# Kernel optimization log

Measured on AMD Instinct MI355X. Metric: run time of the kernel, lower is better.

## Reference

```python
import jax, jax.numpy as jnp
import numpy as np

N = 50000      # nodes
E = 800000     # edges
D = 96         # nfeat
C = 40         # nclass
NITE = 8       # train_nite / eval_nite
SMOOTH = 0.5   # smooth_fac


def setup_inputs() -> dict:
    key = jax.random.key(0)
    ks = jax.random.split(key, 6)
    x = jax.random.normal(ks[0], (N, D), dtype=jnp.float32)
    edge_row = jax.random.randint(ks[1], (E,), 0, N)
    edge_col = jax.random.randint(ks[2], (E,), 0, N)
    # ~1/avg_degree scale mimics a symmetrically normalized adjacency
    edge_vals = jax.random.uniform(ks[3], (E,), dtype=jnp.float32) / 16.0
    W_gc = jax.random.normal(ks[4], (D, D), dtype=jnp.float32) / jnp.sqrt(jnp.float32(D))
    b_gc = jnp.zeros((D,), dtype=jnp.float32)
    W_lin = jax.random.normal(ks[5], (D, C), dtype=jnp.float32) / jnp.sqrt(jnp.float32(D))
    return {"x": x, "edge_row": edge_row, "edge_col": edge_col,
            "edge_vals": edge_vals, "W_gc": W_gc, "b_gc": b_gc, "W_lin": W_lin}


def reference(x, edge_row, edge_col, edge_vals, W_gc, b_gc, W_lin):
    # One iteration: GraphConvolution (support = h @ W; out = A @ support + b),
    # smoothing skip connection, ReLU. Dropout is identity (eval / rate 0).
    def one_iter(h, _):
        support = h @ W_gc                                   # [N, D]
        msg = support[edge_col] * edge_vals[:, None]         # [E, D] gather + scale
        agg = jax.ops.segment_sum(msg, edge_row, num_segments=N) + b_gc  # [N, D]
        h_new = jax.nn.relu(SMOOTH * h + (1.0 - SMOOTH) * agg)
        return h_new, None

    h, _ = jax.lax.scan(one_iter, x, None, length=NITE)
    logits = h @ W_lin                                       # [N, C]
    return jax.nn.log_softmax(logits, axis=1)
```

## Files before the change

### kernel.cpp

```cpp
#include <hip/hip_runtime.h>

#define N_NODES 50000
#define E_EDGES 800000
#define D_FEAT  96
#define C_CLS   40
#define N_ITER  8

#define SCAN_CHUNK 1024
#define SCAN_NB ((N_NODES + SCAN_CHUNK - 1) / SCAN_CHUNK)

typedef short bf16x8 __attribute__((ext_vector_type(8)));
typedef float f32x4  __attribute__((ext_vector_type(4)));
typedef float f32x2  __attribute__((ext_vector_type(2)));

#if defined(__has_builtin)
#if __has_builtin(__builtin_amdgcn_cvt_pk_f32_fp8) && __has_builtin(__builtin_amdgcn_cvt_pk_fp8_f32)
#define HAVE_FP8_CVT 1
#endif
#endif
#ifndef HAVE_FP8_CVT
#define HAVE_FP8_CVT 0
#endif

static __device__ __forceinline__ unsigned short f2bf(float f) {
    unsigned u = __float_as_uint(f);
    u = (u + 0x7FFF + ((u >> 16) & 1)) >> 16;
    return (unsigned short)u;
}

static __device__ __forceinline__ unsigned f32_to_fp8_manual(float f) {
    unsigned u = __float_as_uint(f);
    unsigned s = u >> 31;
    int e8 = (int)((u >> 23) & 0xFF) - 127 + 7;
    unsigned m23 = u & 0x7FFFFF;
    if (e8 <= 0) return s << 7;
    if (e8 >= 15) return (s << 7) | 0x7E;
    unsigned m = m23 >> 20;
    unsigned rem = m23 & 0xFFFFF;
    if (rem > 0x80000u || (rem == 0x80000u && (m & 1))) {
        m++;
        if (m == 8) { m = 0; e8++; if (e8 >= 15) return (s << 7) | 0x7E; }
    }
    return (s << 7) | ((unsigned)e8 << 3) | m;
}
static __device__ __forceinline__ float fp8_to_f32_manual(unsigned b) {
    unsigned s = (b >> 7) & 1, e = (b >> 3) & 0xF, m = b & 7;
    if (e == 0) return 0.0f;
    return __uint_as_float((s << 31) | ((e + 120) << 23) | (m << 20));
}

static __device__ __forceinline__ void fp8x4_dec(unsigned w, float* o) {
#if HAVE_FP8_CVT
    f32x2 lo = __builtin_amdgcn_cvt_pk_f32_fp8(w, false);
    f32x2 hi = __builtin_amdgcn_cvt_pk_f32_fp8(w, true);
    o[0] = lo[0]; o[1] = lo[1]; o[2] = hi[0]; o[3] = hi[1];
#else
    o[0] = fp8_to_f32_manual(w & 0xFF);
    o[1] = fp8_to_f32_manual((w >> 8) & 0xFF);
    o[2] = fp8_to_f32_manual((w >> 16) & 0xFF);
    o[3] = fp8_to_f32_manual((w >> 24) & 0xFF);
#endif
}
static __device__ __forceinline__ unsigned fp8x4_enc(float a, float b, float c, float d) {
#if HAVE_FP8_CVT
    unsigned w = __builtin_amdgcn_cvt_pk_fp8_f32(a, b, 0, false);
    w = __builtin_amdgcn_cvt_pk_fp8_f32(c, d, (int)w, true);
    return w;
#else
    return f32_to_fp8_manual(a) | (f32_to_fp8_manual(b) << 8) |
           (f32_to_fp8_manual(c) << 16) | (f32_to_fp8_manual(d) << 24);
#endif
}

__global__ __launch_bounds__(256) void k_hist(const int* __restrict__ erow,
                                              int* __restrict__ deg) {
    int e = blockIdx.x * 256 + threadIdx.x;
    if (e >= E_EDGES) return;
    atomicAdd(&deg[erow[e]], 1);
}

__global__ __launch_bounds__(256) void k_scan_reduce(const int* __restrict__ deg,
                                                     int* __restrict__ bsum) {
    __shared__ int sbuf[256];
    int tid = threadIdx.x;
    int base = blockIdx.x * SCAN_CHUNK + tid * 4;
    int s = 0;
    #pragma unroll
    for (int j = 0; j < 4; ++j) {
        int idx = base + j;
        if (idx < N_NODES) s += deg[idx];
    }
    sbuf[tid] = s;
    __syncthreads();
    for (int d = 128; d > 0; d >>= 1) {
        if (tid < d) sbuf[tid] += sbuf[tid + d];
        __syncthreads();
    }
    if (tid == 0) bsum[blockIdx.x] = sbuf[0];
}

__global__ __launch_bounds__(64) void k_scan_tops(int* __restrict__ bsum) {
    int lane = threadIdx.x;
    int v = (lane < SCAN_NB) ? bsum[lane] : 0;
    int inc = v;
    #pragma unroll
    for (int d = 1; d < 64; d <<= 1) {
        int up = __shfl_up(inc, d, 64);
        if (lane >= d) inc += up;
    }
    if (lane < SCAN_NB) bsum[lane] = inc - v;
}

__global__ __launch_bounds__(256) void k_scan_add(const int* __restrict__ deg,
                                                  const int* __restrict__ bsum_ex,
                                                  int* __restrict__ off,
                                                  int* __restrict__ cursor) {
    __shared__ int sbuf[256];
    int tid = threadIdx.x;
    int base = blockIdx.x * SCAN_CHUNK + tid * 4;
    int v[4];
    int s = 0;
    #pragma unroll
    for (int j = 0; j < 4; ++j) {
        int idx = base + j;
        v[j] = (idx < N_NODES) ? deg[idx] : 0;
        s += v[j];
    }
    sbuf[tid] = s;
    __syncthreads();
    for (int d = 1; d < 256; d <<= 1) {
        int t = (tid >= d) ? sbuf[tid - d] : 0;
        __syncthreads();
        sbuf[tid] += t;
        __syncthreads();
    }
    int ex = bsum_ex[blockIdx.x] + sbuf[tid] - s;
    #pragma unroll
    for (int j = 0; j < 4; ++j) {
        int idx = base + j;
        if (idx < N_NODES) {
            off[idx] = ex;
            cursor[idx] = ex;
            ex += v[j];
        }
    }
    if (blockIdx.x == 0 && tid == 0) off[N_NODES] = E_EDGES;
}

__global__ __launch_bounds__(256) void k_build(const int* __restrict__ erow,
                                               const int* __restrict__ ecol,
                                               const float* __restrict__ eval_,
                                               int* __restrict__ cursor,
                                               unsigned* __restrict__ epk) {
    int e = blockIdx.x * 256 + threadIdx.x;
    if (e >= E_EDGES) return;
    int r = erow[e];
    int pos = atomicAdd(&cursor[r], 1);
    unsigned pk = (unsigned)(ecol[e] & 0xFFFF) | ((unsigned)f2bf(eval_[e]) << 16);
    epk[pos] = pk;
}

__global__ __launch_bounds__(256) void k_prep_w(const float* __restrict__ W,
                                                unsigned short* __restrict__ WB) {
    for (int idx = threadIdx.x; idx < 18 * 64; idx += 256) {
        int grp = idx >> 6;
        int lane = idx & 63;
        int t = grp / 3, s = grp - t * 3;
        int n = t * 16 + (lane & 15);
        int k0 = s * 32 + (lane >> 4) * 8;
        unsigned short* dst = WB + (size_t)idx * 8;
        #pragma unroll
        for (int j = 0; j < 8; ++j)
            dst[j] = f2bf(W[(k0 + j) * D_FEAT + n]);
    }
}

__global__ __launch_bounds__(256) void k_cvt_bf16(const float* __restrict__ src,
                                                  unsigned short* __restrict__ dst,
                                                  int n8) {
    int g = blockIdx.x * 256 + threadIdx.x;
    if (g >= n8) return;
    const float4* s4 = (const float4*)src + (size_t)g * 2;
    float4 x0 = s4[0], x1 = s4[1];
    float vals[8] = {x0.x, x0.y, x0.z, x0.w, x1.x, x1.y, x1.z, x1.w};
    uint4 pk; unsigned* pku = (unsigned*)&pk;
    #pragma unroll
    for (int w2 = 0; w2 < 4; ++w2) {
        unsigned lo = f2bf(vals[w2 * 2 + 0]);
        unsigned hi = f2bf(vals[w2 * 2 + 1]);
        pku[w2] = lo | (hi << 16);
    }
    *(uint4*)(dst + (size_t)g * 8) = pk;
}

__global__ __launch_bounds__(256) void k_matmul_mfma(
        const unsigned short* __restrict__ hb,
        const unsigned short* __restrict__ WB,
        unsigned char* __restrict__ support) {
    __shared__ float sm[64 * 100];
    int tid = threadIdx.x;
    int wave = tid >> 6, lane = tid & 63;
    int q = lane >> 4, c = lane & 15;
    int m0 = blockIdx.x * 64 + wave * 16;

    if (m0 < N_NODES) {
        const unsigned short* arow = hb + (size_t)(m0 + c) * D_FEAT + q * 8;
        bf16x8 a0 = *(const bf16x8*)(arow);
        bf16x8 a1 = *(const bf16x8*)(arow + 32);
        bf16x8 a2 = *(const bf16x8*)(arow + 64);
        #pragma unroll
        for (int t = 0; t < 6; ++t) {
            const unsigned short* bp = WB + ((size_t)(t * 3) * 64 + lane) * 8;
            bf16x8 b0 = *(const bf16x8*)(bp);
            bf16x8 b1 = *(const bf16x8*)(bp + 64 * 8);
            bf16x8 b2 = *(const bf16x8*)(bp + 128 * 8);
            f32x4 acc = {0.f, 0.f, 0.f, 0.f};
            acc = __builtin_amdgcn_mfma_f32_16x16x32_bf16(a0, b0, acc, 0, 0, 0);
            acc = __builtin_amdgcn_mfma_f32_16x16x32_bf16(a1, b1, acc, 0, 0, 0);
            acc = __builtin_amdgcn_mfma_f32_16x16x32_bf16(a2, b2, acc, 0, 0, 0);
            #pragma unroll
            for (int r = 0; r < 4; ++r)
                sm[(wave * 16 + q * 4 + r) * 100 + t * 16 + c] = acc[r];
        }
    }
    __syncthreads();

    #pragma unroll
    for (int oo = 0; oo < 3; ++oo) {
        int o = tid + oo * 256;
        int row = o / 12;
        int cb = (o - row * 12) * 8;
        int grow = blockIdx.x * 64 + row;
        if (grow < N_NODES) {
            const float* sp = sm + row * 100 + cb;
            uint2 pk;
            pk.x = fp8x4_enc(sp[0], sp[1], sp[2], sp[3]);
            pk.y = fp8x4_enc(sp[4], sp[5], sp[6], sp[7]);
            *(uint2*)(support + (size_t)grow * D_FEAT + cb) = pk;
        }
    }
}

__global__ __launch_bounds__(192) void k_agg(const int* __restrict__ off,
                                             const unsigned* __restrict__ epk,
                                             const unsigned char* __restrict__ support,
                                             const unsigned short* hin,
                                             const float* __restrict__ b,
                                             unsigned short* hout) {
    int gid = blockIdx.x * 192 + threadIdx.x;
    int n = gid / 12;
    int q = gid % 12;
    if (n >= N_NODES) return;

    int s = off[n];
    int e = off[n + 1];

    float acc[8];
    #pragma unroll
    for (int j = 0; j < 8; ++j) acc[j] = 0.0f;

    int i = s;
    for (; i < e && (i & 3); ++i) {
        unsigned p = epk[i];
        float v = __uint_as_float(p & 0xFFFF0000u);
        uint2 r = *(const uint2*)(support + (size_t)(p & 0xFFFFu) * D_FEAT + q * 8);
        float f[8];
        fp8x4_dec(r.x, f);
        fp8x4_dec(r.y, f + 4);
        #pragma unroll
        for (int j = 0; j < 8; ++j) acc[j] = fmaf(f[j], v, acc[j]);
    }
    for (; i + 4 <= e; i += 4) {
        uint4 pq = *(const uint4*)(epk + i);
        const unsigned* pp = (const unsigned*)&pq;
        uint2 r0 = *(const uint2*)(support + (size_t)(pp[0] & 0xFFFFu) * D_FEAT + q * 8);
        uint2 r1 = *(const uint2*)(support + (size_t)(pp[1] & 0xFFFFu) * D_FEAT + q * 8);
        uint2 r2 = *(const uint2*)(support + (size_t)(pp[2] & 0xFFFFu) * D_FEAT + q * 8);
        uint2 r3 = *(const uint2*)(support + (size_t)(pp[3] & 0xFFFFu) * D_FEAT + q * 8);
        float v0 = __uint_as_float(pp[0] & 0xFFFF0000u);
        float v1 = __uint_as_float(pp[1] & 0xFFFF0000u);
        float v2 = __uint_as_float(pp[2] & 0xFFFF0000u);
        float v3 = __uint_as_float(pp[3] & 0xFFFF0000u);
        float f0[8], f1[8], f2[8], f3[8];
        fp8x4_dec(r0.x, f0); fp8x4_dec(r0.y, f0 + 4);
        fp8x4_dec(r1.x, f1); fp8x4_dec(r1.y, f1 + 4);
        fp8x4_dec(r2.x, f2); fp8x4_dec(r2.y, f2 + 4);
        fp8x4_dec(r3.x, f3); fp8x4_dec(r3.y, f3 + 4);
        #pragma unroll
        for (int j = 0; j < 8; ++j) {
            acc[j] = fmaf(f0[j], v0, acc[j]);
            acc[j] = fmaf(f1[j], v1, acc[j]);
            acc[j] = fmaf(f2[j], v2, acc[j]);
            acc[j] = fmaf(f3[j], v3, acc[j]);
        }
    }
    for (; i < e; ++i) {
        unsigned p = epk[i];
        float v = __uint_as_float(p & 0xFFFF0000u);
        uint2 r = *(const uint2*)(support + (size_t)(p & 0xFFFFu) * D_FEAT + q * 8);
        float f[8];
        fp8x4_dec(r.x, f);
        fp8x4_dec(r.y, f + 4);
        #pragma unroll
        for (int j = 0; j < 8; ++j) acc[j] = fmaf(f[j], v, acc[j]);
    }

    uint4 hq = *(const uint4*)(hin + (size_t)n * D_FEAT + q * 8);
    const unsigned* hu = (const unsigned*)&hq;
    const float* brow = b + q * 8;
    float og[8];
    #pragma unroll
    for (int w2 = 0; w2 < 4; ++w2) {
        float h0 = __uint_as_float(hu[w2] << 16);
        float h1 = __uint_as_float(hu[w2] & 0xFFFF0000u);
        og[w2*2+0] = fmaxf(0.5f * h0 + 0.5f * (acc[w2*2+0] + brow[w2*2+0]), 0.0f);
        og[w2*2+1] = fmaxf(0.5f * h1 + 0.5f * (acc[w2*2+1] + brow[w2*2+1]), 0.0f);
    }
    uint4 pk; unsigned* pku = (unsigned*)&pk;
    #pragma unroll
    for (int w2 = 0; w2 < 4; ++w2) {
        unsigned lo = f2bf(og[w2 * 2 + 0]);
        unsigned hi = f2bf(og[w2 * 2 + 1]);
        pku[w2] = lo | (hi << 16);
    }
    *(uint4*)(hout + (size_t)n * D_FEAT + q * 8) = pk;
}

__global__ __launch_bounds__(256) void k_final(const unsigned short* __restrict__ hb,
                                               const float* __restrict__ Wg,
                                               float* __restrict__ out) {
    __shared__ float Wl[D_FEAT * C_CLS];
    {
        const float4* src = (const float4*)Wg;
        float4* dst = (float4*)Wl;
        for (int i = threadIdx.x; i < 960; i += 256) dst[i] = src[i];
    }
    __syncthreads();

    int n = blockIdx.x * 256 + threadIdx.x;
    if (n >= N_NODES) return;

    float acc[C_CLS];
    #pragma unroll
    for (int c = 0; c < C_CLS; ++c) acc[c] = 0.0f;

    const unsigned short* hrow = hb + (size_t)n * D_FEAT;
    for (int g = 0; g < 12; ++g) {
        uint4 hq = *(const uint4*)(hrow + g * 8);
        const unsigned* hu = (const unsigned*)&hq;
        float hv[8];
        #pragma unroll
        for (int w2 = 0; w2 < 4; ++w2) {
            hv[w2*2+0] = __uint_as_float(hu[w2] << 16);
            hv[w2*2+1] = __uint_as_float(hu[w2] & 0xFFFF0000u);
        }
        #pragma unroll
        for (int kk = 0; kk < 8; ++kk) {
            float hs = hv[kk];
            const float* wr = &Wl[(g * 8 + kk) * C_CLS];
            #pragma unroll
            for (int c4 = 0; c4 < 10; ++c4) {
                float4 w = *(const float4*)(wr + c4 * 4);
                acc[c4 * 4 + 0] = fmaf(hs, w.x, acc[c4 * 4 + 0]);
                acc[c4 * 4 + 1] = fmaf(hs, w.y, acc[c4 * 4 + 1]);
                acc[c4 * 4 + 2] = fmaf(hs, w.z, acc[c4 * 4 + 2]);
                acc[c4 * 4 + 3] = fmaf(hs, w.w, acc[c4 * 4 + 3]);
            }
        }
    }

    float m = acc[0];
    #pragma unroll
    for (int c = 1; c < C_CLS; ++c) m = fmaxf(m, acc[c]);
    float s = 0.0f;
    #pragma unroll
    for (int c = 0; c < C_CLS; ++c) s += expf(acc[c] - m);
    float lse = m + logf(s);

    float* orow = out + (size_t)n * C_CLS;
    #pragma unroll
    for (int c4 = 0; c4 < 10; ++c4)
        *(float4*)(orow + c4 * 4) =
            make_float4(acc[c4 * 4 + 0] - lse, acc[c4 * 4 + 1] - lse,
                        acc[c4 * 4 + 2] - lse, acc[c4 * 4 + 3] - lse);
}

static inline size_t align256(size_t x) { return (x + 255) & ~(size_t)255; }

extern "C" void kernel_launch(void* const* d_in, const int* in_sizes, int n_in,
                              void* d_out, int out_size, void* d_ws, size_t ws_size,
                              hipStream_t stream) {
    const float* x    = (const float*)d_in[0];
    const int*   erow = (const int*)  d_in[1];
    const int*   ecol = (const int*)  d_in[2];
    const float* ev   = (const float*)d_in[3];
    const float* Wgc  = (const float*)d_in[4];
    const float* bgc  = (const float*)d_in[5];
    const float* Wlin = (const float*)d_in[6];
    float* out = (float*)d_out;

    const size_t NF = (size_t)N_NODES * D_FEAT;
    char* ws = (char*)d_ws;
    unsigned short* hb         = (unsigned short*)ws; ws += align256(NF * 2);
    unsigned short* xb         = (unsigned short*)ws; ws += align256(NF * 2);
    unsigned char*  support_f8 = (unsigned char*)ws;  ws += align256(NF);
    unsigned*       epk        = (unsigned*)ws;       ws += align256((size_t)E_EDGES * 4);
    unsigned short* WB         = (unsigned short*)ws; ws += align256((size_t)18 * 64 * 8 * 2);
    int*            off        = (int*)ws;            ws += align256((size_t)(N_NODES + 1) * 4);
    int*            deg        = (int*)ws;            ws += align256((size_t)N_NODES * 4);
    int*            cursor     = (int*)ws;            ws += align256((size_t)N_NODES * 4);
    int*            bsum       = (int*)ws;            ws += align256((size_t)SCAN_NB * 4);

    hipMemsetAsync(deg, 0, (size_t)N_NODES * 4, stream);
    k_prep_w     <<<1, 256, 0, stream>>>(Wgc, WB);
    k_cvt_bf16   <<<(int)((NF / 8 + 255) / 256), 256, 0, stream>>>(x, xb, (int)(NF / 8));
    k_hist       <<<(E_EDGES + 255) / 256, 256, 0, stream>>>(erow, deg);
    k_scan_reduce<<<SCAN_NB, 256, 0, stream>>>(deg, bsum);
    k_scan_tops  <<<1, 64, 0, stream>>>(bsum);
    k_scan_add   <<<SCAN_NB, 256, 0, stream>>>(deg, bsum, off, cursor);
    k_build      <<<(E_EDGES + 255) / 256, 256, 0, stream>>>(erow, ecol, ev, cursor, epk);

    const int g_mm = (N_NODES + 63) / 64;
    const int g_ag = (N_NODES * 12 + 191) / 192;
    for (int it = 0; it < N_ITER; ++it) {
        const unsigned short* hin = (it == 0) ? xb : hb;
        k_matmul_mfma<<<g_mm, 256, 0, stream>>>(hin, WB, support_f8);
        k_agg        <<<g_ag, 192, 0, stream>>>(off, epk, support_f8, hin, bgc, hb);
    }
    k_final<<<(N_NODES + 255) / 256, 256, 0, stream>>>(hb, Wlin, out);
}
```

Measured before the change: 442.7 us.

## Sort nodes by degree for aggregation and widen per-thread feature slice to 16

Adds a degree histogram, scan and scatter that build a permutation grouping nodes of equal in-degree, so wavefronts in the aggregation kernel process nodes with similar edge counts and diverge less. The aggregation kernel now uses 6 threads per node, each loading 16 fp8 features per edge with 128-bit loads instead of 8 with 64-bit loads. This halves the edge-index loads per node and lowers the thread count, but adds three small setup kernels, an indirection through perm, and writes that no longer follow node order.

```diff
diff --git a/kernel.cpp b/kernel.cpp
--- a/kernel.cpp
+++ b/kernel.cpp
@@ -8,6 +8,7 @@
 
 #define SCAN_CHUNK 1024
 #define SCAN_NB ((N_NODES + SCAN_CHUNK - 1) / SCAN_CHUNK)
+#define DBINS 64
 
 typedef short bf16x8 __attribute__((ext_vector_type(8)));
 typedef float f32x4  __attribute__((ext_vector_type(4)));
@@ -48,7 +49,6 @@
     if (e == 0) return 0.0f;
     return __uint_as_float((s << 31) | ((e + 120) << 23) | (m << 20));
 }
-
 static __device__ __forceinline__ void fp8x4_dec(unsigned w, float* o) {
 #if HAVE_FP8_CVT
     f32x2 lo = __builtin_amdgcn_cvt_pk_f32_fp8(w, false);
@@ -114,9 +114,12 @@
 __global__ __launch_bounds__(256) void k_scan_add(const int* __restrict__ deg,
                                                   const int* __restrict__ bsum_ex,
                                                   int* __restrict__ off,
-                                                  int* __restrict__ cursor) {
+                                                  int* __restrict__ cursor,
+                                                  int* __restrict__ dh) {
     __shared__ int sbuf[256];
+    __shared__ int lh[DBINS];
     int tid = threadIdx.x;
+    if (tid < DBINS) lh[tid] = 0;
     int base = blockIdx.x * SCAN_CHUNK + tid * 4;
     int v[4];
     int s = 0;
@@ -142,9 +145,34 @@
             off[idx] = ex;
             cursor[idx] = ex;
             ex += v[j];
+            atomicAdd(&lh[min(v[j], DBINS - 1)], 1);
         }
     }
     if (blockIdx.x == 0 && tid == 0) off[N_NODES] = E_EDGES;
+    __syncthreads();
+    if (tid < DBINS && lh[tid] != 0) atomicAdd(&dh[tid], lh[tid]);
+}
+
+__global__ __launch_bounds__(64) void k_dscan(int* __restrict__ dh) {
+    int lane = threadIdx.x;
+    int v = dh[lane];
+    int inc = v;
+    #pragma unroll
+    for (int d = 1; d < 64; d <<= 1) {
+        int up = __shfl_up(inc, d, 64);
+        if (lane >= d) inc += up;
+    }
+    dh[lane] = inc - v;
+}
+
+__global__ __launch_bounds__(256) void k_dscatter(const int* __restrict__ deg,
+                                                  int* __restrict__ dh,
+                                                  int* __restrict__ perm) {
+    int n = blockIdx.x * 256 + threadIdx.x;
+    if (n >= N_NODES) return;
+    int d = min(deg[n], DBINS - 1);
+    int pos = atomicAdd(&dh[d], 1);
+    perm[pos] = n;
 }
 
 __global__ __launch_bounds__(256) void k_build(const int* __restrict__ erow,
@@ -242,88 +270,105 @@
 }
 
 __global__ __launch_bounds__(192) void k_agg(const int* __restrict__ off,
+                                             const int* __restrict__ perm,
                                              const unsigned* __restrict__ epk,
                                              const unsigned char* __restrict__ support,
                                              const unsigned short* hin,
                                              const float* __restrict__ b,
                                              unsigned short* hout) {
     int gid = blockIdx.x * 192 + threadIdx.x;
-    int n = gid / 12;
-    int q = gid % 12;
-    if (n >= N_NODES) return;
+    int ni = gid / 6;
+    int q = gid % 6;
+    if (ni >= N_NODES) return;
+    int n = perm[ni];
 
     int s = off[n];
     int e = off[n + 1];
 
-    float acc[8];
-    #pragma unroll
-    for (int j = 0; j < 8; ++j) acc[j] = 0.0f;
+    float acc[16];
+    #pragma unroll
+    for (int j = 0; j < 16; ++j) acc[j] = 0.0f;
 
     int i = s;
     for (; i < e && (i & 3); ++i) {
         unsigned p = epk[i];
         float v = __uint_as_float(p & 0xFFFF0000u);
-        uint2 r = *(const uint2*)(support + (size_t)(p & 0xFFFFu) * D_FEAT + q * 8);
-        float f[8];
-        fp8x4_dec(r.x, f);
-        fp8x4_dec(r.y, f + 4);
-        #pragma unroll
-        for (int j = 0; j < 8; ++j) acc[j] = fmaf(f[j], v, acc[j]);
+        uint4 r = *(const uint4*)(support + (size_t)(p & 0xFFFFu) * D_FEAT + q * 16);
+        float f[16];
+        fp8x4_dec(r.x, f); fp8x4_dec(r.y, f + 4);
+        fp8x4_dec(r.z, f + 8); fp8x4_dec(r.w, f + 12);
+        #pragma unroll
+        for (int j = 0; j < 16; ++j) acc[j] = fmaf(f[j], v, acc[j]);
     }
     for (; i + 4 <= e; i += 4) {
         uint4 pq = *(const uint4*)(epk + i);
         const unsigned* pp = (const unsigned*)&pq;
-        uint2 r0 = *(const uint2*)(support + (size_t)(pp[0] & 0xFFFFu) * D_FEAT + q * 8);
-        uint2 r1 = *(const uint2*)(support + (size_t)(pp[1] & 0xFFFFu) * D_FEAT + q * 8);
-        uint2 r2 = *(const uint2*)(support + (size_t)(pp[2] & 0xFFFFu) * D_FEAT + q * 8);
-        uint2 r3 = *(const uint2*)(support + (size_t)(pp[3] & 0xFFFFu) * D_FEAT + q * 8);
+        uint4 r0 = *(const uint4*)(support + (size_t)(pp[0] & 0xFFFFu) * D_FEAT + q * 16);
+        uint4 r1 = *(const uint4*)(support + (size_t)(pp[1] & 0xFFFFu) * D_FEAT + q * 16);
+        uint4 r2 = *(const uint4*)(support + (size_t)(pp[2] & 0xFFFFu) * D_FEAT + q * 16);
+        uint4 r3 = *(const uint4*)(support + (size_t)(pp[3] & 0xFFFFu) * D_FEAT + q * 16);
         float v0 = __uint_as_float(pp[0] & 0xFFFF0000u);
         float v1 = __uint_as_float(pp[1] & 0xFFFF0000u);
         float v2 = __uint_as_float(pp[2] & 0xFFFF0000u);
         float v3 = __uint_as_float(pp[3] & 0xFFFF0000u);
-        float f0[8], f1[8], f2[8], f3[8];
-        fp8x4_dec(r0.x, f0); fp8x4_dec(r0.y, f0 + 4);
-        fp8x4_dec(r1.x, f1); fp8x4_dec(r1.y, f1 + 4);
-        fp8x4_dec(r2.x, f2); fp8x4_dec(r2.y, f2 + 4);
-        fp8x4_dec(r3.x, f3); fp8x4_dec(r3.y, f3 + 4);
-        #pragma unroll
-        for (int j = 0; j < 8; ++j) {
-            acc[j] = fmaf(f0[j], v0, acc[j]);
-            acc[j] = fmaf(f1[j], v1, acc[j]);
-            acc[j] = fmaf(f2[j], v2, acc[j]);
-            acc[j] = fmaf(f3[j], v3, acc[j]);
-        }
+        float f[16];
+        fp8x4_dec(r0.x, f); fp8x4_dec(r0.y, f + 4);
+        fp8x4_dec(r0.z, f + 8); fp8x4_dec(r0.w, f + 12);
+        #pragma unroll
+        for (int j = 0; j < 16; ++j) acc[j] = fmaf(f[j], v0, acc[j]);
+        fp8x4_dec(r1.x, f); fp8x4_dec(r1.y, f + 4);
+        fp8x4_dec(r1.z, f + 8); fp8x4_dec(r1.w, f + 12);
+        #pragma unroll
+        for (int j = 0; j < 16; ++j) acc[j] = fmaf(f[j], v1, acc[j]);
+        fp8x4_dec(r2.x, f); fp8x4_dec(r2.y, f + 4);
+        fp8x4_dec(r2.z, f + 8); fp8x4_dec(r2.w, f + 12);
+        #pragma unroll
+        for (int j = 0; j < 16; ++j) acc[j] = fmaf(f[j], v2, acc[j]);
+        fp8x4_dec(r3.x, f); fp8x4_dec(r3.y, f + 4);
+        fp8x4_dec(r3.z, f + 8); fp8x4_dec(r3.w, f + 12);
+        #pragma unroll
+        for (int j = 0; j < 16; ++j) acc[j] = fmaf(f[j], v3, acc[j]);
     }
     for (; i < e; ++i) {
         unsigned p = epk[i];
         float v = __uint_as_float(p & 0xFFFF0000u);
-        uint2 r = *(const uint2*)(support + (size_t)(p & 0xFFFFu) * D_FEAT + q * 8);
-        float f[8];
-        fp8x4_dec(r.x, f);
-        fp8x4_dec(r.y, f + 4);
-        #pragma unroll
-        for (int j = 0; j < 8; ++j) acc[j] = fmaf(f[j], v, acc[j]);
-    }
-
-    uint4 hq = *(const uint4*)(hin + (size_t)n * D_FEAT + q * 8);
-    const unsigned* hu = (const unsigned*)&hq;
-    const float* brow = b + q * 8;
-    float og[8];
+        uint4 r = *(const uint4*)(support + (size_t)(p & 0xFFFFu) * D_FEAT + q * 16);
+        float f[16];
+        fp8x4_dec(r.x, f); fp8x4_dec(r.y, f + 4);
+        fp8x4_dec(r.z, f + 8); fp8x4_dec(r.w, f + 12);
+        #pragma unroll
+        for (int j = 0; j < 16; ++j) acc[j] = fmaf(f[j], v, acc[j]);
+    }
+
+    const unsigned short* hrow = hin + (size_t)n * D_FEAT + q * 16;
+    uint4 hq0 = *(const uint4*)(hrow);
+    uint4 hq1 = *(const uint4*)(hrow + 8);
+    const unsigned* hu0 = (const unsigned*)&hq0;
+    const unsigned* hu1 = (const unsigned*)&hq1;
+    const float* brow = b + q * 16;
+    float og[16];
     #pragma unroll
     for (int w2 = 0; w2 < 4; ++w2) {
-        float h0 = __uint_as_float(hu[w2] << 16);
-        float h1 = __uint_as_float(hu[w2] & 0xFFFF0000u);
+        float h0 = __uint_as_float(hu0[w2] << 16);
+        float h1 = __uint_as_float(hu0[w2] & 0xFFFF0000u);
         og[w2*2+0] = fmaxf(0.5f * h0 + 0.5f * (acc[w2*2+0] + brow[w2*2+0]), 0.0f);
         og[w2*2+1] = fmaxf(0.5f * h1 + 0.5f * (acc[w2*2+1] + brow[w2*2+1]), 0.0f);
-    }
-    uint4 pk; unsigned* pku = (unsigned*)&pk;
+        float h2 = __uint_as_float(hu1[w2] << 16);
+        float h3 = __uint_as_float(hu1[w2] & 0xFFFF0000u);
+        og[8+w2*2+0] = fmaxf(0.5f * h2 + 0.5f * (acc[8+w2*2+0] + brow[8+w2*2+0]), 0.0f);
+        og[8+w2*2+1] = fmaxf(0.5f * h3 + 0.5f * (acc[8+w2*2+1] + brow[8+w2*2+1]), 0.0f);
+    }
+    uint4 pk0, pk1;
+    unsigned* pu0 = (unsigned*)&pk0;
+    unsigned* pu1 = (unsigned*)&pk1;
     #pragma unroll
     for (int w2 = 0; w2 < 4; ++w2) {
-        unsigned lo = f2bf(og[w2 * 2 + 0]);
-        unsigned hi = f2bf(og[w2 * 2 + 1]);
-        pku[w2] = lo | (hi << 16);
-    }
-    *(uint4*)(hout + (size_t)n * D_FEAT + q * 8) = pk;
+        pu0[w2] = (unsigned)f2bf(og[w2*2+0]) | ((unsigned)f2bf(og[w2*2+1]) << 16);
+        pu1[w2] = (unsigned)f2bf(og[8+w2*2+0]) | ((unsigned)f2bf(og[8+w2*2+1]) << 16);
+    }
+    unsigned short* orow = hout + (size_t)n * D_FEAT + q * 16;
+    *(uint4*)(orow) = pk0;
+    *(uint4*)(orow + 8) = pk1;
 }
 
 __global__ __launch_bounds__(256) void k_final(const unsigned short* __restrict__ hb,
@@ -407,25 +452,29 @@
     unsigned*       epk        = (unsigned*)ws;       ws += align256((size_t)E_EDGES * 4);
     unsigned short* WB         = (unsigned short*)ws; ws += align256((size_t)18 * 64 * 8 * 2);
     int*            off        = (int*)ws;            ws += align256((size_t)(N_NODES + 1) * 4);
-    int*            deg        = (int*)ws;            ws += align256((size_t)N_NODES * 4);
+    int*            perm       = (int*)ws;            ws += align256((size_t)N_NODES * 4);
     int*            cursor     = (int*)ws;            ws += align256((size_t)N_NODES * 4);
     int*            bsum       = (int*)ws;            ws += align256((size_t)SCAN_NB * 4);
-
-    hipMemsetAsync(deg, 0, (size_t)N_NODES * 4, stream);
+    int*            deg        = (int*)ws;            ws += align256((size_t)N_NODES * 4);
+    int*            dh         = (int*)ws;            ws += align256((size_t)DBINS * 4);
+
+    hipMemsetAsync(deg, 0, align256((size_t)N_NODES * 4) + (size_t)DBINS * 4, stream);
     k_prep_w     <<<1, 256, 0, stream>>>(Wgc, WB);
     k_cvt_bf16   <<<(int)((NF / 8 + 255) / 256), 256, 0, stream>>>(x, xb, (int)(NF / 8));
     k_hist       <<<(E_EDGES + 255) / 256, 256, 0, stream>>>(erow, deg);
     k_scan_reduce<<<SCAN_NB, 256, 0, stream>>>(deg, bsum);
     k_scan_tops  <<<1, 64, 0, stream>>>(bsum);
-    k_scan_add   <<<SCAN_NB, 256, 0, stream>>>(deg, bsum, off, cursor);
+    k_scan_add   <<<SCAN_NB, 256, 0, stream>>>(deg, bsum, off, cursor, dh);
+    k_dscan      <<<1, 64, 0, stream>>>(dh);
+    k_dscatter   <<<(N_NODES + 255) / 256, 256, 0, stream>>>(deg, dh, perm);
     k_build      <<<(E_EDGES + 255) / 256, 256, 0, stream>>>(erow, ecol, ev, cursor, epk);
 
     const int g_mm = (N_NODES + 63) / 64;
-    const int g_ag = (N_NODES * 12 + 191) / 192;
+    const int g_ag = (N_NODES * 6 + 191) / 192;
     for (int it = 0; it < N_ITER; ++it) {
         const unsigned short* hin = (it == 0) ? xb : hb;
         k_matmul_mfma<<<g_mm, 256, 0, stream>>>(hin, WB, support_f8);
-        k_agg        <<<g_ag, 192, 0, stream>>>(off, epk, support_f8, hin, bgc, hb);
+        k_agg        <<<g_ag, 192, 0, stream>>>(off, perm, epk, support_f8, hin, bgc, hb);
     }
     k_final<<<(N_NODES + 255) / 256, 256, 0, stream>>>(hb, Wlin, out);
 }
```

After: 583.5 us. 1.32x slower.
